# Performance work log

Hardware: AMD Instinct MI355X
Metric: run time of the kernel (lower is better)

## Reference

```python
import jax, jax.numpy as jnp
import numpy as np

N = 100000   # atoms
E = 1600000  # edges (unused by this readout but required by signature)
C = 128      # channel multiplicity of node_feats irreps 128x0e+128x1o
PATH_W = 1.0 / 16.0  # e3nn uvu path weight: sqrt(1/(mul2_path0 + mul2_path1)) = sqrt(1/256)
SQRT3 = float(np.sqrt(3.0))


def setup_inputs() -> dict:
    key = jax.random.key(0)
    ks = jax.random.split(key, 32)
    r = lambda k, s, sc=1.0: jax.random.normal(k, s, dtype=jnp.float32) * sc
    z = lambda s: jnp.zeros(s, dtype=jnp.float32)
    return {
        # forward args
        "node_attrs": r(ks[0], (N, 10)),
        "node_feats": r(ks[1], (N, 4 * C)),           # 128x0e (128) + 128x1o (384)
        "edge_attrs": r(ks[2], (E, 9)),
        "edge_feats": r(ks[3], (E, 8)),
        "edge_index": jax.random.randint(ks[4], (2, E), 0, N),
        "field_feats": r(ks[5], (N, 4)),               # 1x0e + 1x1o
        "charges_0": r(ks[6], (N, 1)),
        "charges_induced": r(ks[7], (N, 1)),
        # o3.Linear(charges_irreps -> node_feats_irreps), fan_in=1 -> plain weight
        "Wq0": r(ks[8], (1, C)), "bq": z((C,)),
        # o3.Linear(potential_irreps -> node_feats_irreps)
        "Wv0": r(ks[9], (1, C)), "bv": z((C,)),
        "Wv1": r(ks[10], (1, C)),                      # 1o -> 128x1o path (no bias)
        # SparseUvuTensorProduct weights: path0 (0e x 0e -> 0e), path1 (1o x 1o -> 0e)
        "wq_s": r(ks[11], (C, C)), "wq_v": r(ks[12], (C, C)),
        "wv_s": r(ks[13], (C, C)), "wv_v": r(ks[14], (C, C)),
        # readout MLP [256,128,128,128,1] with SiLU between layers
        "W1": r(ks[15], (2 * C, 128), 1.0 / np.sqrt(2 * C)), "b1": z((128,)),
        "W2": r(ks[16], (128, 128), 1.0 / np.sqrt(128)), "b2": z((128,)),
        "W3": r(ks[17], (128, 128), 1.0 / np.sqrt(128)), "b3": z((128,)),
        "W4": r(ks[18], (128, 1), 1.0 / np.sqrt(128)), "b4": z((1,)),
    }


def _sparse_uvu_tp(x1s, x1v, x2s, x2v, w_s, w_v):
    """uvu TP (128x0e+128x1o) x (128x0e+128x1o) -> 128x0e, both paths to i_out=0.
    x1s/x2s: [N,C], x1v/x2v: [N,C,3]. Avoids the [N,C,C] pair matrix by
    contracting the weight into x2 first."""
    # path 0e x 0e -> 0e (d=1): mixed_bu = x1_bu * sum_v x2_bv w_uv
    out = x1s * (x2s @ w_s.T)
    # path 1o x 1o -> 0e (d=3): mixed_bu = sum_{v,d} x1_bud x2_bvd w_uv / sqrt(3)
    t = jnp.einsum('bvd,uv->bud', x2v, w_v)
    out = out + jnp.sum(x1v * t, axis=-1) / SQRT3
    return PATH_W * out


def reference(node_attrs, node_feats, edge_attrs, edge_feats, edge_index,
              field_feats, charges_0, charges_induced,
              Wq0, bq, Wv0, bv, Wv1,
              wq_s, wq_v, wv_s, wv_v,
              W1, b1, W2, b2, W3, b3, W4, b4):
    n = node_feats.shape[0]
    node_s = node_feats[:, :C]                 # [N,128] scalar block
    node_v = node_feats[:, C:].reshape(n, C, 3)  # [N,128,3] vector block (mul_ir)

    # q branch: linear_up_q(charges_induced + charges_0)
    q_in = charges_induced + charges_0         # [N,1]
    q_up_s = q_in @ Wq0 + bq                   # [N,128]
    q_up_v = jnp.zeros((n, C, 3), node_feats.dtype)  # 1x0e has no path to 128x1o

    # v branch: linear_up_v(field_feats)
    v_up_s = field_feats[:, :1] @ Wv0 + bv                     # [N,128]
    v_up_v = field_feats[:, None, 1:4] * Wv1[0][None, :, None]  # [N,128,3]

    dot_q = _sparse_uvu_tp(node_s, node_v, q_up_s, q_up_v, wq_s, wq_v)  # [N,128]
    dot_v = _sparse_uvu_tp(node_s, node_v, v_up_s, v_up_v, wv_s, wv_v)  # [N,128]

    h = jnp.concatenate([dot_q, dot_v], axis=-1)  # [N,256]
    h = jax.nn.silu(h @ W1 + b1)
    h = jax.nn.silu(h @ W2 + b2)
    h = jax.nn.silu(h @ W3 + b3)
    return h @ W4 + b4                           # [N,1] per-atom energy readout
```

## Files before the change

### kernel.cpp

```cpp
#include <hip/hip_runtime.h>
#include <hip/hip_bf16.h>

typedef __attribute__((ext_vector_type(8))) short short8;
typedef __attribute__((ext_vector_type(4))) float f32x4;

#define PATH_W 0.0625f
#define INV_SQRT3 0.57735026918962576f

typedef const __attribute__((address_space(1))) char gchar;
typedef __attribute__((address_space(3))) char schar;

__device__ __forceinline__ unsigned short f2bf(float f) {
    unsigned int u = __builtin_bit_cast(unsigned int, f);
    u += 0x7FFFu + ((u >> 16) & 1u);
    return (unsigned short)(u >> 16);
}

__device__ __forceinline__ float silu(float x) {
    return x / (1.0f + __expf(-x));
}

__global__ void prep_all(const float* __restrict__ Wq0, const float* __restrict__ bq,
                         const float* __restrict__ Wv0, const float* __restrict__ bv,
                         const float* __restrict__ Wv1, const float* __restrict__ wq_s,
                         const float* __restrict__ wv_s, const float* __restrict__ wv_v,
                         const float* __restrict__ W1, const float* __restrict__ W2,
                         const float* __restrict__ W3, const float* __restrict__ b1,
                         const float* __restrict__ b2, const float* __restrict__ b3,
                         const float* __restrict__ W4, const float* __restrict__ b4,
                         float* __restrict__ vecs, unsigned short* __restrict__ wp) {
    if (blockIdx.x == 0) {
        int u = threadIdx.x;
        float aq = 0.f, bqs = 0.f, av = 0.f, bvs = 0.f, a1 = 0.f;
        for (int v = 0; v < 128; ++v) {
            float rq = wq_s[u * 128 + v];
            float rv = wv_s[u * 128 + v];
            aq  += Wq0[v] * rq;
            bqs += bq[v]  * rq;
            av  += Wv0[v] * rv;
            bvs += bv[v]  * rv;
            a1  += Wv1[v] * wv_v[u * 128 + v];
        }
        vecs[u]        = PATH_W * aq;
        vecs[128 + u]  = PATH_W * bqs;
        vecs[256 + u]  = PATH_W * av;
        vecs[384 + u]  = PATH_W * bvs;
        vecs[512 + u]  = PATH_W * INV_SQRT3 * a1;
        vecs[640 + u]  = b1[u];
        vecs[768 + u]  = b2[u];
        vecs[896 + u]  = b3[u];
        vecs[1024 + u] = W4[u];
        if (u == 0) { vecs[1152] = b4[0]; vecs[1153] = 0.f; vecs[1154] = 0.f; vecs[1155] = 0.f; }
        return;
    }
    int fid  = blockIdx.x - 1;
    int t    = threadIdx.x;
    int lane = t & 63;
    int half = t >> 6;
    int g  = lane >> 4;
    int r  = lane & 15;
    const float* W;
    int row0, col;
    if (fid < 64) {
        int mt = fid >> 3, ks = fid & 7;
        W = W1; col = mt * 16 + r;
        row0 = ks * 32 + g * 8 + half * 4;
    } else {
        int f2 = fid < 96 ? fid - 64 : fid - 96;
        int mt = f2 >> 2, ks = f2 & 3;
        W = fid < 96 ? W2 : W3; col = mt * 16 + r;
        row0 = half * 64 + ks * 16 + g * 4;
    }
    unsigned short* dst = wp + fid * 512 + lane * 8 + half * 4;
    #pragma unroll
    for (int j = 0; j < 4; ++j) dst[j] = f2bf(W[(row0 + j) * 128 + col]);
}

__global__ __launch_bounds__(256, 1) void fused_main(
    const float* __restrict__ nf,
    const float* __restrict__ field,
    const float* __restrict__ c0, const float* __restrict__ ci,
    const float* __restrict__ vecs,
    const unsigned short* __restrict__ wp,
    float* __restrict__ out, int N)
{
    __shared__ __align__(16) char smem[131072];
    __shared__ __align__(16) float vlds[1156];
    const int tid  = threadIdx.x;
    const int wave = tid >> 6;
    const int lane = tid & 63;
    const int g    = lane >> 4;
    const int nl   = lane & 15;
    const int T    = (N + 63) >> 6;
    const char* wpb = (const char*)wp;

    #pragma unroll
    for (int i = 0; i < 32; ++i) {
        int off = (wave * 32 + i) * 1024;
        __builtin_amdgcn_global_load_lds((gchar*)(wpb + off + lane * 16),
                                         (schar*)(smem + off), 16, 0, 0);
    }
    if (wave == 0) {
        #pragma unroll
        for (int i = 0; i < 5; ++i) {
            int idx = lane + 64 * i;
            if (idx < 289)
                reinterpret_cast<f32x4*>(vlds)[idx] =
                    reinterpret_cast<const f32x4*>(vecs)[idx];
        }
    }

    f32x4 hs[8], hv0[8], hv1[8], hv2[8];
    float c0r, cir; f32x4 ffr;

#define SLOT_LOAD(hh_, bs_, bv_) {                                            \
        const int q_ = (hh_) >> 1, h_ = (hh_) & 1;                            \
        hs[hh_]  = *reinterpret_cast<const f32x4*>((bs_) + 128 * q_ + 16 * h_); \
        hv0[hh_] = *reinterpret_cast<const f32x4*>((bv_) + 384 * q_ + 48 * h_); \
        hv1[hh_] = *reinterpret_cast<const f32x4*>((bv_) + 384 * q_ + 48 * h_ + 16); \
        hv2[hh_] = *reinterpret_cast<const f32x4*>((bv_) + 384 * q_ + 48 * h_ + 32); }

    int tile = blockIdx.x;
    {
        int nd0 = tile * 64 + wave * 16 + nl;
        int ndc = nd0 < N ? nd0 : N - 1;
        const char* nrow = (const char*)nf + (size_t)ndc * 2048;
        const char* bs0 = nrow + 32 * g;
        const char* bv0 = nrow + 512 + 96 * g;
        #pragma unroll
        for (int hh = 0; hh < 8; ++hh) SLOT_LOAD(hh, bs0, bv0)
        c0r = c0[ndc]; cir = ci[ndc];
        ffr = reinterpret_cast<const f32x4*>(field)[ndc];
    }

    __syncthreads();

    const f32x4* vl4 = reinterpret_cast<const f32x4*>(vlds);

    for (; tile < T; tile += gridDim.x) {
        const int nd = tile * 64 + wave * 16 + nl;
        const int nt = tile + gridDim.x;
        const bool hasnext = nt < T;

        const char* bsn = nullptr; const char* bvn = nullptr;
        float c0n = 0.f, cin = 0.f; f32x4 ffn = ffr;
        if (hasnext) {
            int ndn = nt * 64 + wave * 16 + nl;
            ndn = ndn < N ? ndn : N - 1;
            const char* nrow = (const char*)nf + (size_t)ndn * 2048;
            bsn = nrow + 32 * g;
            bvn = nrow + 512 + 96 * g;
            c0n = c0[ndn]; cin = ci[ndn];
            ffn = reinterpret_cast<const f32x4*>(field)[ndn];
        }

        const float q_in = c0r + cir;
        const f32x4 ff   = ffr;

        f32x4 acc[8];
        #pragma unroll
        for (int mt = 0; mt < 8; ++mt) acc[mt] = vl4[160 + mt * 4 + g];

        short8 hfA, hfB;
        #pragma unroll
        for (int q = 0; q < 4; ++q) {
            #pragma unroll
            for (int h = 0; h < 2; ++h) {
                const int hh = 2 * q + h;
                const int m  = 8 * q + 2 * g + h;
                f32x4 aq = vl4[m], bqv = vl4[32 + m], av = vl4[64 + m],
                      bvv = vl4[96 + m], a1 = vl4[128 + m];
                f32x4 s = hs[hh], va = hv0[hh], vb = hv1[hh], vc = hv2[hh];
                float d3[4];
                d3[0] = fmaf(va[0], ff[1], fmaf(va[1], ff[2], va[2] * ff[3]));
                d3[1] = fmaf(va[3], ff[1], fmaf(vb[0], ff[2], vb[1] * ff[3]));
                d3[2] = fmaf(vb[2], ff[1], fmaf(vb[3], ff[2], vc[0] * ff[3]));
                d3[3] = fmaf(vc[1], ff[1], fmaf(vc[2], ff[2], vc[3] * ff[3]));
                #pragma unroll
                for (int j = 0; j < 4; ++j) {
                    float hq = s[j] * fmaf(q_in, aq[j], bqv[j]);
                    float hv = fmaf(s[j], fmaf(ff[0], av[j], bvv[j]), a1[j] * d3[j]);
                    if (h == 0) { hfA[j]     = (short)f2bf(hq); hfB[j]     = (short)f2bf(hv); }
                    else        { hfA[4 + j] = (short)f2bf(hq); hfB[4 + j] = (short)f2bf(hv); }
                }
                __builtin_amdgcn_sched_barrier(0);
                if (hasnext) SLOT_LOAD(hh, bsn, bvn)
            }
            #pragma unroll
            for (int mt = 0; mt < 8; ++mt) {
                short8 a0 = *reinterpret_cast<const short8*>(
                    smem + (mt * 8 + q) * 1024 + lane * 16);
                acc[mt] = __builtin_amdgcn_mfma_f32_16x16x32_bf16(a0, hfA, acc[mt], 0, 0, 0);
                short8 a4 = *reinterpret_cast<const short8*>(
                    smem + (mt * 8 + q + 4) * 1024 + lane * 16);
                acc[mt] = __builtin_amdgcn_mfma_f32_16x16x32_bf16(a4, hfB, acc[mt], 0, 0, 0);
            }
        }

        short8 hf2[4];
        #pragma unroll
        for (int ks = 0; ks < 4; ++ks)
            #pragma unroll
            for (int hp = 0; hp < 2; ++hp)
                #pragma unroll
                for (int j = 0; j < 4; ++j)
                    hf2[ks][hp * 4 + j] = (short)f2bf(silu(acc[hp * 4 + ks][j]));

        f32x4 acc2[8];
        #pragma unroll
        for (int mt = 0; mt < 8; ++mt) acc2[mt] = vl4[192 + mt * 4 + g];
        #pragma unroll
        for (int ks = 0; ks < 4; ++ks) {
            #pragma unroll
            for (int mt = 0; mt < 8; ++mt) {
                short8 a = *reinterpret_cast<const short8*>(
                    smem + 65536 + (mt * 4 + ks) * 1024 + lane * 16);
                acc2[mt] = __builtin_amdgcn_mfma_f32_16x16x32_bf16(a, hf2[ks], acc2[mt], 0, 0, 0);
            }
        }

        short8 hf3[4];
        #pragma unroll
        for (int ks = 0; ks < 4; ++ks)
            #pragma unroll
            for (int hp = 0; hp < 2; ++hp)
                #pragma unroll
                for (int j = 0; j < 4; ++j)
                    hf3[ks][hp * 4 + j] = (short)f2bf(silu(acc2[hp * 4 + ks][j]));

        f32x4 acc3[8];
        #pragma unroll
        for (int mt = 0; mt < 8; ++mt) acc3[mt] = vl4[224 + mt * 4 + g];
        #pragma unroll
        for (int ks = 0; ks < 4; ++ks) {
            #pragma unroll
            for (int mt = 0; mt < 8; ++mt) {
                short8 a = *reinterpret_cast<const short8*>(
                    smem + 98304 + (mt * 4 + ks) * 1024 + lane * 16);
                acc3[mt] = __builtin_amdgcn_mfma_f32_16x16x32_bf16(a, hf3[ks], acc3[mt], 0, 0, 0);
            }
        }

        float acc_out = 0.f;
        #pragma unroll
        for (int mt = 0; mt < 8; ++mt) {
            f32x4 w4v = vl4[256 + mt * 4 + g];
            acc_out += silu(acc3[mt][0]) * w4v[0];
            acc_out += silu(acc3[mt][1]) * w4v[1];
            acc_out += silu(acc3[mt][2]) * w4v[2];
            acc_out += silu(acc3[mt][3]) * w4v[3];
        }
        acc_out += __shfl_xor(acc_out, 16, 64);
        acc_out += __shfl_xor(acc_out, 32, 64);
        if (g == 0 && nd < N) out[nd] = acc_out + vlds[1152];

        c0r = c0n; cir = cin; ffr = ffn;
    }
#undef SLOT_LOAD
}

extern "C" void kernel_launch(void* const* d_in, const int* in_sizes, int n_in,
                              void* d_out, int out_size, void* d_ws, size_t ws_size,
                              hipStream_t stream) {
    const float* node_feats = (const float*)d_in[1];
    const float* field      = (const float*)d_in[5];
    const float* c0         = (const float*)d_in[6];
    const float* ci         = (const float*)d_in[7];
    const float* Wq0        = (const float*)d_in[8];
    const float* bq         = (const float*)d_in[9];
    const float* Wv0        = (const float*)d_in[10];
    const float* bv         = (const float*)d_in[11];
    const float* Wv1        = (const float*)d_in[12];
    const float* wq_s       = (const float*)d_in[13];
    const float* wv_s       = (const float*)d_in[15];
    const float* wv_v       = (const float*)d_in[16];
    const float* W1         = (const float*)d_in[17];
    const float* b1         = (const float*)d_in[18];
    const float* W2         = (const float*)d_in[19];
    const float* b2         = (const float*)d_in[20];
    const float* W3         = (const float*)d_in[21];
    const float* b3         = (const float*)d_in[22];
    const float* W4         = (const float*)d_in[23];
    const float* b4         = (const float*)d_in[24];

    const int N = in_sizes[1] / 512;
    float* vecs = (float*)d_ws;
    unsigned short* wp = (unsigned short*)((char*)d_ws + 8192);

    prep_all<<<129, 128, 0, stream>>>(Wq0, bq, Wv0, bv, Wv1, wq_s, wv_s, wv_v,
                                      W1, W2, W3, b1, b2, b3, W4, b4, vecs, wp);
    const int T = (N + 63) / 64;
    const int blocks = T < 256 ? T : 256;
    fused_main<<<blocks, 256, 0, stream>>>(node_feats, field, c0, ci, vecs, wp,
                                           (float*)d_out, N);
}
```

Measured before the change: 77.88 us.

## Double block to 8 waves and halve per-thread prefetch register buffer

The fused kernel now runs 512 threads (8 waves) per block, each block covering 128 nodes. The staging of the packed weights into shared memory is split across twice as many waves. The input prefetch buffer is halved from 8 to 4 slots per thread. The second half of the current node row is loaded mid-iteration, and only the first half of the next tile is prefetched. This cuts register pressure so twice the waves can hide memory latency, at the cost of less prefetch distance for the second half of each row.

```diff
diff --git a/kernel.cpp b/kernel.cpp
--- a/kernel.cpp
+++ b/kernel.cpp
@@ -76,7 +76,7 @@
     for (int j = 0; j < 4; ++j) dst[j] = f2bf(W[(row0 + j) * 128 + col]);
 }
 
-__global__ __launch_bounds__(256, 1) void fused_main(
+__global__ __launch_bounds__(512, 1) void fused_main(
     const float* __restrict__ nf,
     const float* __restrict__ field,
     const float* __restrict__ c0, const float* __restrict__ ci,
@@ -91,12 +91,12 @@
     const int lane = tid & 63;
     const int g    = lane >> 4;
     const int nl   = lane & 15;
-    const int T    = (N + 63) >> 6;
+    const int T    = (N + 127) >> 7;
     const char* wpb = (const char*)wp;
 
     #pragma unroll
-    for (int i = 0; i < 32; ++i) {
-        int off = (wave * 32 + i) * 1024;
+    for (int i = 0; i < 16; ++i) {
+        int off = (wave * 16 + i) * 1024;
         __builtin_amdgcn_global_load_lds((gchar*)(wpb + off + lane * 16),
                                          (schar*)(smem + off), 16, 0, 0);
     }
@@ -110,25 +110,28 @@
         }
     }
 
-    f32x4 hs[8], hv0[8], hv1[8], hv2[8];
+    f32x4 hs[4], hv0[4], hv1[4], hv2[4];
     float c0r, cir; f32x4 ffr;
-
-#define SLOT_LOAD(hh_, bs_, bv_) {                                            \
-        const int q_ = (hh_) >> 1, h_ = (hh_) & 1;                            \
-        hs[hh_]  = *reinterpret_cast<const f32x4*>((bs_) + 128 * q_ + 16 * h_); \
-        hv0[hh_] = *reinterpret_cast<const f32x4*>((bv_) + 384 * q_ + 48 * h_); \
-        hv1[hh_] = *reinterpret_cast<const f32x4*>((bv_) + 384 * q_ + 48 * h_ + 16); \
-        hv2[hh_] = *reinterpret_cast<const f32x4*>((bv_) + 384 * q_ + 48 * h_ + 32); }
+    const char* bsr; const char* bvr;
+
+#define SLOT_LOAD(sl_, q_, h_, bs_, bv_) {                                    \
+        hs[sl_]  = *reinterpret_cast<const f32x4*>((bs_) + 128 * (q_) + 16 * (h_)); \
+        hv0[sl_] = *reinterpret_cast<const f32x4*>((bv_) + 384 * (q_) + 48 * (h_)); \
+        hv1[sl_] = *reinterpret_cast<const f32x4*>((bv_) + 384 * (q_) + 48 * (h_) + 16); \
+        hv2[sl_] = *reinterpret_cast<const f32x4*>((bv_) + 384 * (q_) + 48 * (h_) + 32); }
 
     int tile = blockIdx.x;
     {
-        int nd0 = tile * 64 + wave * 16 + nl;
+        int nd0 = tile * 128 + wave * 16 + nl;
         int ndc = nd0 < N ? nd0 : N - 1;
         const char* nrow = (const char*)nf + (size_t)ndc * 2048;
-        const char* bs0 = nrow + 32 * g;
-        const char* bv0 = nrow + 512 + 96 * g;
-        #pragma unroll
-        for (int hh = 0; hh < 8; ++hh) SLOT_LOAD(hh, bs0, bv0)
+        bsr = nrow + 32 * g;
+        bvr = nrow + 512 + 96 * g;
+        #pragma unroll
+        for (int qh = 0; qh < 2; ++qh)
+            #pragma unroll
+            for (int h = 0; h < 2; ++h)
+                SLOT_LOAD(2 * qh + h, qh, h, bsr, bvr)
         c0r = c0[ndc]; cir = ci[ndc];
         ffr = reinterpret_cast<const f32x4*>(field)[ndc];
     }
@@ -138,14 +141,14 @@
     const f32x4* vl4 = reinterpret_cast<const f32x4*>(vlds);
 
     for (; tile < T; tile += gridDim.x) {
-        const int nd = tile * 64 + wave * 16 + nl;
+        const int nd = tile * 128 + wave * 16 + nl;
         const int nt = tile + gridDim.x;
         const bool hasnext = nt < T;
 
-        const char* bsn = nullptr; const char* bvn = nullptr;
+        const char* bsn = bsr; const char* bvn = bvr;
         float c0n = 0.f, cin = 0.f; f32x4 ffn = ffr;
         if (hasnext) {
-            int ndn = nt * 64 + wave * 16 + nl;
+            int ndn = nt * 128 + wave * 16 + nl;
             ndn = ndn < N ? ndn : N - 1;
             const char* nrow = (const char*)nf + (size_t)ndn * 2048;
             bsn = nrow + 32 * g;
@@ -163,37 +166,45 @@
 
         short8 hfA, hfB;
         #pragma unroll
-        for (int q = 0; q < 4; ++q) {
-            #pragma unroll
-            for (int h = 0; h < 2; ++h) {
-                const int hh = 2 * q + h;
-                const int m  = 8 * q + 2 * g + h;
-                f32x4 aq = vl4[m], bqv = vl4[32 + m], av = vl4[64 + m],
-                      bvv = vl4[96 + m], a1 = vl4[128 + m];
-                f32x4 s = hs[hh], va = hv0[hh], vb = hv1[hh], vc = hv2[hh];
-                float d3[4];
-                d3[0] = fmaf(va[0], ff[1], fmaf(va[1], ff[2], va[2] * ff[3]));
-                d3[1] = fmaf(va[3], ff[1], fmaf(vb[0], ff[2], vb[1] * ff[3]));
-                d3[2] = fmaf(vb[2], ff[1], fmaf(vb[3], ff[2], vc[0] * ff[3]));
-                d3[3] = fmaf(vc[1], ff[1], fmaf(vc[2], ff[2], vc[3] * ff[3]));
+        for (int half = 0; half < 2; ++half) {
+            #pragma unroll
+            for (int qh = 0; qh < 2; ++qh) {
+                const int q = 2 * half + qh;
                 #pragma unroll
-                for (int j = 0; j < 4; ++j) {
-                    float hq = s[j] * fmaf(q_in, aq[j], bqv[j]);
-                    float hv = fmaf(s[j], fmaf(ff[0], av[j], bvv[j]), a1[j] * d3[j]);
-                    if (h == 0) { hfA[j]     = (short)f2bf(hq); hfB[j]     = (short)f2bf(hv); }
-                    else        { hfA[4 + j] = (short)f2bf(hq); hfB[4 + j] = (short)f2bf(hv); }
+                for (int h = 0; h < 2; ++h) {
+                    const int slot = 2 * qh + h;
+                    const int m = 8 * q + 2 * g + h;
+                    f32x4 aq = vl4[m], bqv = vl4[32 + m], av = vl4[64 + m],
+                          bvv = vl4[96 + m], a1 = vl4[128 + m];
+                    f32x4 s = hs[slot], va = hv0[slot], vb = hv1[slot], vc = hv2[slot];
+                    float d3[4];
+                    d3[0] = fmaf(va[0], ff[1], fmaf(va[1], ff[2], va[2] * ff[3]));
+                    d3[1] = fmaf(va[3], ff[1], fmaf(vb[0], ff[2], vb[1] * ff[3]));
+                    d3[2] = fmaf(vb[2], ff[1], fmaf(vb[3], ff[2], vc[0] * ff[3]));
+                    d3[3] = fmaf(vc[1], ff[1], fmaf(vc[2], ff[2], vc[3] * ff[3]));
+                    #pragma unroll
+                    for (int j = 0; j < 4; ++j) {
+                        float hq = s[j] * fmaf(q_in, aq[j], bqv[j]);
+                        float hv = fmaf(s[j], fmaf(ff[0], av[j], bvv[j]), a1[j] * d3[j]);
+                        if (h == 0) { hfA[j]     = (short)f2bf(hq); hfB[j]     = (short)f2bf(hv); }
+                        else        { hfA[4 + j] = (short)f2bf(hq); hfB[4 + j] = (short)f2bf(hv); }
+                    }
+                    __builtin_amdgcn_sched_barrier(0);
+                    if (half == 0) {
+                        SLOT_LOAD(slot, qh + 2, h, bsr, bvr)
+                    } else if (hasnext) {
+                        SLOT_LOAD(slot, qh, h, bsn, bvn)
+                    }
                 }
-                __builtin_amdgcn_sched_barrier(0);
-                if (hasnext) SLOT_LOAD(hh, bsn, bvn)
-            }
-            #pragma unroll
-            for (int mt = 0; mt < 8; ++mt) {
-                short8 a0 = *reinterpret_cast<const short8*>(
-                    smem + (mt * 8 + q) * 1024 + lane * 16);
-                acc[mt] = __builtin_amdgcn_mfma_f32_16x16x32_bf16(a0, hfA, acc[mt], 0, 0, 0);
-                short8 a4 = *reinterpret_cast<const short8*>(
-                    smem + (mt * 8 + q + 4) * 1024 + lane * 16);
-                acc[mt] = __builtin_amdgcn_mfma_f32_16x16x32_bf16(a4, hfB, acc[mt], 0, 0, 0);
+                #pragma unroll
+                for (int mt = 0; mt < 8; ++mt) {
+                    short8 a0 = *reinterpret_cast<const short8*>(
+                        smem + (mt * 8 + q) * 1024 + lane * 16);
+                    acc[mt] = __builtin_amdgcn_mfma_f32_16x16x32_bf16(a0, hfA, acc[mt], 0, 0, 0);
+                    short8 a4 = *reinterpret_cast<const short8*>(
+                        smem + (mt * 8 + q + 4) * 1024 + lane * 16);
+                    acc[mt] = __builtin_amdgcn_mfma_f32_16x16x32_bf16(a4, hfB, acc[mt], 0, 0, 0);
+                }
             }
         }
 
@@ -254,6 +265,7 @@
         acc_out += __shfl_xor(acc_out, 32, 64);
         if (g == 0 && nd < N) out[nd] = acc_out + vlds[1152];
 
+        bsr = bsn; bvr = bvn;
         c0r = c0n; cir = cin; ffr = ffn;
     }
 #undef SLOT_LOAD
@@ -289,8 +301,8 @@
 
     prep_all<<<129, 128, 0, stream>>>(Wq0, bq, Wv0, bv, Wv1, wq_s, wv_s, wv_v,
                                       W1, W2, W3, b1, b2, b3, W4, b4, vecs, wp);
-    const int T = (N + 63) / 64;
+    const int T = (N + 127) / 128;
     const int blocks = T < 256 ? T : 256;
-    fused_main<<<blocks, 256, 0, stream>>>(node_feats, field, c0, ci, vecs, wp,
+    fused_main<<<blocks, 512, 0, stream>>>(node_feats, field, c0, ci, vecs, wp,
                                            (float*)d_out, N);
 }
```

Result: faster. 73.98 us (-5.0%).
